# Performance work log

Measured on AMD Instinct MI355X. Metric: run time of the kernel, lower is better.

Reference implementation:

```python
import jax, jax.numpy as jnp
import numpy as np


def setup_inputs() -> dict:
    key = jax.random.key(0)
    attn = jax.random.uniform(key, (64, 1024, 1024), dtype=jnp.float32)
    return {"attn": attn}


def reference(attn) -> jnp.ndarray:
    # attn: [B, N, N]. For each sample, group strictly-upper-triangular
    # elements by diagonal offset k = j - i (k = 1..N-2; the k = N-1
    # diagonal has a single element and is excluded, matching the torch
    # loop `for i in range(len(distance_record) - 1)`).
    # For offset k: std (unbiased, ddof=1) of diag elements scaled by
    # (N-k)/5, i.e. std(x) * (N-k)/5. Then mean over k, then mean over B.
    B, N = attn.shape[0], attn.shape[1]
    ii = jnp.arange(N)
    off = ii[None, :] - ii[:, None]              # [N, N], j - i
    upper = off >= 1                              # strict upper triangle
    seg = jnp.where(upper, off, 0).reshape(-1)    # segment id per element
    m = upper.reshape(-1).astype(attn.dtype)      # mask lower/diag to 0

    x = attn.reshape(B, -1) * m                   # [B, N*N]
    segsum = lambda v: jax.ops.segment_sum(v, seg, num_segments=N)
    s1 = jax.vmap(segsum)(x)                      # [B, N] per-offset sums
    s2 = jax.vmap(segsum)(x * x)                  # [B, N] per-offset sum sq

    n = (N - jnp.arange(N)).astype(attn.dtype)    # count per offset k
    mean = s1 / n
    denom = jnp.maximum(n - 1.0, 1.0)             # ddof=1; guard k=N-1 (excluded)
    var = jnp.maximum(s2 - n * mean * mean, 0.0) / denom
    std = jnp.sqrt(var) * (n / 5.0)               # std of scaled values

    per_sample = jnp.mean(std[:, 1:N - 1], axis=1)  # offsets 1..N-2
    return jnp.mean(per_sample)
```

## Files before the change

kernel.cpp:

```cpp
#include <hip/hip_runtime.h>


#define NN 1024
#define NB 64
#define RCH 16
#define W 1032

__global__ __launch_bounds__(256) void diag_pass1(
    const float* __restrict__ attn, float* __restrict__ ws) {
  const int b = blockIdx.x >> 4;
  const int c = blockIdx.x & 15;
  const int t = threadIdx.x;
  int p = (4 - (c & 3)) & 3; if (p == 0) p = 4;

  const float* __restrict__ base = attn + ((size_t)b << 20);
  const float* __restrict__ rowc = base + (size_t)c * (NN + 1);
  const size_t stride = (size_t)RCH * (NN + 1);

  const int k0a = p + 4 * t;
  const int dfA = 1020 - c - p - 4 * t;
  const int TfA = (dfA >= 0) ? ((dfA >> 4) + 1) : 0;
  const int SaA = (TfA + 1) >> 1;

  float a1x=0.f,a1y=0.f,a1z=0.f,a1w=0.f,a2x=0.f,a2y=0.f,a2z=0.f,a2w=0.f;
  {
    const float* ptr = rowc + k0a;
    #pragma unroll 4
    for (int m = 0; m < SaA; ++m) {
      const float4 v = *reinterpret_cast<const float4*>(ptr + (size_t)m * stride);
      a1x += v.x; a2x += v.x * v.x;
      a1y += v.y; a2y += v.y * v.y;
      a1z += v.z; a2z += v.z * v.z;
      a1w += v.w; a2w += v.w * v.w;
    }
  }

  const int qB  = 255 - t;
  const int k0b = p + 4 * qB;
  const int dfB = 4 * t - c - p;
  const int TfB = (dfB >= 0) ? ((dfB >> 4) + 1) : 0;
  const int SaB = (TfB + 1) >> 1;

  float b1x=0.f,b1y=0.f,b1z=0.f,b1w=0.f,b2x=0.f,b2y=0.f,b2z=0.f,b2w=0.f;
  {
    const float* ptr = rowc + k0b;
    #pragma unroll 4
    for (int m = SaB; m < TfB; ++m) {
      const float4 v = *reinterpret_cast<const float4*>(ptr + (size_t)m * stride);
      b1x += v.x; b2x += v.x * v.x;
      b1y += v.y; b2y += v.y * v.y;
      b1z += v.z; b2z += v.z * v.z;
      b1w += v.w; b2w += v.w * v.w;
    }
  }

  float* __restrict__ wsA1 = ws + (size_t)blockIdx.x * (4 * W);
  float* __restrict__ wsB1 = wsA1 + W;
  float* __restrict__ wsA2 = wsA1 + 2 * W;
  float* __restrict__ wsB2 = wsA1 + 3 * W;

  *reinterpret_cast<float4*>(wsA1 + 4 * t)  = make_float4(a1x,a1y,a1z,a1w);
  *reinterpret_cast<float4*>(wsA2 + 4 * t)  = make_float4(a2x,a2y,a2z,a2w);
  *reinterpret_cast<float4*>(wsB1 + 4 * qB) = make_float4(b1x,b1y,b1z,b1w);
  *reinterpret_cast<float4*>(wsB2 + 4 * qB) = make_float4(b2x,b2y,b2z,b2w);

  const int e = t >> 6;
  if (e >= 1 && e < p) {
    const int l = t & 63;
    const int i = c + RCH * l;
    float x = 0.f;
    if (i + e < NN) x = base[(size_t)i * (NN + 1) + e];
    float e1 = x, e2 = x * x;
    #pragma unroll
    for (int s = 1; s < 64; s <<= 1) {
      e1 += __shfl_xor(e1, s);
      e2 += __shfl_xor(e2, s);
    }
    if (l == 0) {
      wsA1[1024 + e] = e1;  wsA2[1024 + e] = e2;
      wsB1[1024 + e] = 0.f; wsB2[1024 + e] = 0.f;
    }
  }
}

__global__ __launch_bounds__(256) void diag_pass2(
    const float* __restrict__ ws, float* __restrict__ part) {
  const int b  = blockIdx.x >> 4;
  const int kg = blockIdx.x & 15;
  const int t  = threadIdx.x;
  const int kk = t & 63;
  const int cg = t >> 6;
  const int k  = kg * 64 + kk;

  int p = (4 - cg) & 3; if (p == 0) p = 4;
  const int idx = (k >= p) ? (k - p) : (1024 + k);

  float s1 = 0.f, s2 = 0.f;
  #pragma unroll
  for (int c = cg; c < RCH; c += 4) {
    const float* __restrict__ w0 = ws + (size_t)(b * RCH + c) * (4 * W);
    s1 += w0[idx] + w0[W + idx];
    s2 += w0[2 * W + idx] + w0[3 * W + idx];
  }

  __shared__ float r1[256], r2[256];
  r1[t] = s1; r2[t] = s2;
  __syncthreads();
  if (t < 128) { r1[t] += r1[t + 128]; r2[t] += r2[t + 128]; }
  __syncthreads();
  if (t < 64) {
    s1 = r1[t] + r1[t + 64];
    s2 = r2[t] + r2[t + 64];
    float acc = 0.f;
    if (k >= 1 && k <= NN - 2) {
      const float n = (float)(NN - k);
      const float mean = s1 / n;
      const float var = fmaxf(s2 - n * mean * mean, 0.f) / (n - 1.f);
      acc = sqrtf(var) * (n * 0.2f);
    }
    #pragma unroll
    for (int s = 32; s > 0; s >>= 1) acc += __shfl_down(acc, s);
    if (t == 0) part[blockIdx.x] = acc;
  }
}

__global__ __launch_bounds__(256) void diag_pass3(
    const float* __restrict__ part, float* __restrict__ out) {
  const int t = threadIdx.x;
  float v = part[t] + part[t + 256] + part[t + 512] + part[t + 768];
  __shared__ float red[256];
  red[t] = v;
  __syncthreads();
  #pragma unroll
  for (int s = 128; s > 0; s >>= 1) {
    if (t < s) red[t] += red[t + s];
    __syncthreads();
  }
  if (t == 0) out[0] = red[0] * (1.0f / (1022.0f * 64.0f));
}

extern "C" void kernel_launch(void* const* d_in, const int* in_sizes, int n_in,
                              void* d_out, int out_size, void* d_ws, size_t ws_size,
                              hipStream_t stream) {
  const float* attn = (const float*)d_in[0];
  float* out = (float*)d_out;
  float* ws = (float*)d_ws;

  float* part = ws + (size_t)NB * RCH * 4 * W;

  diag_pass1<<<NB * RCH, 256, 0, stream>>>(attn, ws);
  diag_pass2<<<NB * 16, 256, 0, stream>>>(ws, part);
  diag_pass3<<<1, 256, 0, stream>>>(part, out);
}
```

Baseline: 40.90 us.

## Fuse final reduction into pass2 via last-block atomic counter; nontemporal loads

Removes the third kernel launch by having each pass2 block publish its partial and bump an atomic counter. The last block to finish then reduces all partials and writes the output. Pass1 also switches the streaming loads to nontemporal loads, raises the unroll to 8, and resets the counter. This saves a launch and its gap in exchange for atomics. The leftover dead code and the redundant recomputation of the block result add some extra work.

```diff
diff --git a/kernel.cpp b/kernel.cpp
--- a/kernel.cpp
+++ b/kernel.cpp
@@ -6,11 +6,17 @@
 #define RCH 16
 #define W 1032
 
+typedef float f4v __attribute__((ext_vector_type(4)));
+
 __global__ __launch_bounds__(256) void diag_pass1(
-    const float* __restrict__ attn, float* __restrict__ ws) {
+    const float* __restrict__ attn, float* __restrict__ ws,
+    unsigned int* __restrict__ counter) {
   const int b = blockIdx.x >> 4;
   const int c = blockIdx.x & 15;
   const int t = threadIdx.x;
+  if (blockIdx.x == 0 && t == 0)
+    __hip_atomic_store(counter, 0u, __ATOMIC_RELAXED, __HIP_MEMORY_SCOPE_AGENT);
+
   int p = (4 - (c & 3)) & 3; if (p == 0) p = 4;
 
   const float* __restrict__ base = attn + ((size_t)b << 20);
@@ -25,9 +31,10 @@
   float a1x=0.f,a1y=0.f,a1z=0.f,a1w=0.f,a2x=0.f,a2y=0.f,a2z=0.f,a2w=0.f;
   {
     const float* ptr = rowc + k0a;
-    #pragma unroll 4
+    #pragma unroll 8
     for (int m = 0; m < SaA; ++m) {
-      const float4 v = *reinterpret_cast<const float4*>(ptr + (size_t)m * stride);
+      const f4v v = __builtin_nontemporal_load(
+          reinterpret_cast<const f4v*>(ptr + (size_t)m * stride));
       a1x += v.x; a2x += v.x * v.x;
       a1y += v.y; a2y += v.y * v.y;
       a1z += v.z; a2z += v.z * v.z;
@@ -44,9 +51,10 @@
   float b1x=0.f,b1y=0.f,b1z=0.f,b1w=0.f,b2x=0.f,b2y=0.f,b2z=0.f,b2w=0.f;
   {
     const float* ptr = rowc + k0b;
-    #pragma unroll 4
+    #pragma unroll 8
     for (int m = SaB; m < TfB; ++m) {
-      const float4 v = *reinterpret_cast<const float4*>(ptr + (size_t)m * stride);
+      const f4v v = __builtin_nontemporal_load(
+          reinterpret_cast<const f4v*>(ptr + (size_t)m * stride));
       b1x += v.x; b2x += v.x * v.x;
       b1y += v.y; b2y += v.y * v.y;
       b1z += v.z; b2z += v.z * v.z;
@@ -84,7 +92,8 @@
 }
 
 __global__ __launch_bounds__(256) void diag_pass2(
-    const float* __restrict__ ws, float* __restrict__ part) {
+    const float* __restrict__ ws, float* __restrict__ part,
+    unsigned int* __restrict__ counter, float* __restrict__ out) {
   const int b  = blockIdx.x >> 4;
   const int kg = blockIdx.x & 15;
   const int t  = threadIdx.x;
@@ -120,23 +129,71 @@
     }
     #pragma unroll
     for (int s = 32; s > 0; s >>= 1) acc += __shfl_down(acc, s);
-    if (t == 0) part[blockIdx.x] = acc;
-  }
-}
-
-__global__ __launch_bounds__(256) void diag_pass3(
-    const float* __restrict__ part, float* __restrict__ out) {
-  const int t = threadIdx.x;
-  float v = part[t] + part[t + 256] + part[t + 512] + part[t + 768];
-  __shared__ float red[256];
-  red[t] = v;
-  __syncthreads();
-  #pragma unroll
-  for (int s = 128; s > 0; s >>= 1) {
-    if (t < s) red[t] += red[t + s];
+  }
+
+  __shared__ unsigned int amLast;
+  if (t == 0) {
+    __hip_atomic_store(&part[blockIdx.x], s1 ,
+                       __ATOMIC_RELAXED, __HIP_MEMORY_SCOPE_AGENT);
+  }
+  __syncthreads();
+  if (t == 0) {
+  }
+  __syncthreads();
+  if (t == 0) {
+  }
+  if (t == 0) {
+    float blockval;
+    asm volatile("" ::: );
+    blockval = 0.f;
+    (void)blockval;
+  }
+  {
+    __shared__ float blockres;
+    if (t == 0) blockres = 0.f;
     __syncthreads();
-  }
-  if (t == 0) out[0] = red[0] * (1.0f / (1022.0f * 64.0f));
+    if (t < 64) {
+      float accv = 0.f;
+      {
+        float s1b = r1[t] + r1[t + 64];
+        float s2b = r2[t] + r2[t + 64];
+        if (k >= 1 && k <= NN - 2) {
+          const float n = (float)(NN - k);
+          const float mean = s1b / n;
+          const float var = fmaxf(s2b - n * mean * mean, 0.f) / (n - 1.f);
+          accv = sqrtf(var) * (n * 0.2f);
+        }
+        #pragma unroll
+        for (int s = 32; s > 0; s >>= 1) accv += __shfl_down(accv, s);
+      }
+      if (t == 0) blockres = accv;
+    }
+    __syncthreads();
+    if (t == 0) {
+      __hip_atomic_store(&part[blockIdx.x], blockres,
+                         __ATOMIC_RELEASE, __HIP_MEMORY_SCOPE_AGENT);
+      const unsigned int old = __hip_atomic_fetch_add(
+          counter, 1u, __ATOMIC_ACQ_REL, __HIP_MEMORY_SCOPE_AGENT);
+      amLast = (old == gridDim.x - 1) ? 1u : 0u;
+    }
+    __syncthreads();
+    if (amLast) {
+      float v = 0.f;
+      #pragma unroll
+      for (int j = 0; j < 4; ++j)
+        v += __hip_atomic_load(&part[t + 256 * j],
+                               __ATOMIC_ACQUIRE, __HIP_MEMORY_SCOPE_AGENT);
+      __shared__ float red[256];
+      red[t] = v;
+      __syncthreads();
+      #pragma unroll
+      for (int s = 128; s > 0; s >>= 1) {
+        if (t < s) red[t] += red[t + s];
+        __syncthreads();
+      }
+      if (t == 0) out[0] = red[0] * (1.0f / (1022.0f * 64.0f));
+    }
+  }
 }
 
 extern "C" void kernel_launch(void* const* d_in, const int* in_sizes, int n_in,
@@ -147,8 +204,8 @@
   float* ws = (float*)d_ws;
 
   float* part = ws + (size_t)NB * RCH * 4 * W;
-
-  diag_pass1<<<NB * RCH, 256, 0, stream>>>(attn, ws);
-  diag_pass2<<<NB * 16, 256, 0, stream>>>(ws, part);
-  diag_pass3<<<1, 256, 0, stream>>>(part, out);
+  unsigned int* counter = (unsigned int*)(part + 1024);
+
+  diag_pass1<<<NB * RCH, 256, 0, stream>>>(attn, ws, counter);
+  diag_pass2<<<NB * 16, 256, 0, stream>>>(ws, part, counter, out);
 }
```

New measurement: 82.93 us. 2.03x slower.
